# Optimization experiments

Hardware: AMD Instinct MI355X
Metric: run time of the kernel (lower is better)

The kernel has to match this reference:

```python
import jax, jax.numpy as jnp
import numpy as np

NUM_GRAPHS = 512

def setup_inputs() -> dict:
    key = jax.random.key(0)
    ks = jax.random.split(key, 6)
    N, E, D = 100000, 1600000, 128
    x = jax.random.normal(ks[0], (N, D), dtype=jnp.float32)
    edge_index = jax.random.randint(ks[1], (2, E), 0, N, dtype=jnp.int64)
    batch = jnp.sort(jax.random.randint(ks[2], (N,), 0, NUM_GRAPHS, dtype=jnp.int64))
    scale = 1.0 / np.sqrt(D)
    Ws = jax.random.normal(ks[3], (4, D, D), dtype=jnp.float32) * scale
    bs = jnp.zeros((4, D), dtype=jnp.float32)
    Wl = jax.random.normal(ks[4], (D, 1), dtype=jnp.float32) * scale
    bl = jnp.zeros((1,), dtype=jnp.float32)
    return {"x": x, "edge_index": edge_index, "batch": batch,
            "Ws": Ws, "bs": bs, "Wl": Wl, "bl": bl}

def reference(x, edge_index, batch, Ws, bs, Wl, bl):
    N = x.shape[0]
    loops = jnp.arange(N, dtype=edge_index.dtype)
    # GCNConv: add self-loops, symmetric normalization D^{-1/2} A D^{-1/2}
    row = jnp.concatenate([edge_index[0], loops])  # source nodes
    col = jnp.concatenate([edge_index[1], loops])  # target nodes
    deg = jax.ops.segment_sum(jnp.ones_like(col, dtype=x.dtype), col, num_segments=N)
    dinv = jnp.where(deg > 0, jax.lax.rsqrt(jnp.maximum(deg, 1.0)), 0.0)
    norm = dinv[row] * dinv[col]  # [E+N]
    h = x
    for i in range(Ws.shape[0]):
        h = h @ Ws[i]                                   # [N, D]
        msg = h[row] * norm[:, None]                    # gather + scale, [E+N, D]
        h = jax.ops.segment_sum(msg, col, num_segments=N) + bs[i]
        h = jax.nn.relu(h)                              # dropout is identity in eval
    # global_mean_pool over graphs
    sums = jax.ops.segment_sum(h, batch, num_segments=NUM_GRAPHS)
    cnt = jax.ops.segment_sum(jnp.ones((N,), h.dtype), batch, num_segments=NUM_GRAPHS)
    pooled = sums / jnp.maximum(cnt, 1.0)[:, None]      # [G, D]
    return pooled @ Wl + bl                             # [G, 1]
```

## Files before the change

kernel.cpp:

```cpp
#include <hip/hip_runtime.h>


constexpr int D = 128;
constexpr int NGRAPH = 512;
constexpr int CHUNK = 4096;
constexpr int BSH = 9;
constexpr int OP = 136;

typedef __attribute__((ext_vector_type(8))) short bf16x8;
typedef __attribute__((ext_vector_type(4))) float f32x4;
typedef int i32x4u __attribute__((ext_vector_type(4), aligned(4)));

__device__ __forceinline__ float bf2f(unsigned short b) {
    return __uint_as_float(((unsigned int)b) << 16);
}
__device__ __forceinline__ unsigned short f2bf(float f) {
    unsigned int u = __float_as_uint(f);
    u += 0x7FFFu + ((u >> 16) & 1u);
    return (unsigned short)(u >> 16);
}

__global__ __launch_bounds__(256) void setup_all(
        const float4* __restrict__ x4, ushort4* __restrict__ hb, int n4, int CB,
        const float* __restrict__ W, unsigned short* __restrict__ Wt,
        const int* __restrict__ ec, int E, int* __restrict__ bucketCnt) {
    __shared__ int h[256];
    const int t = threadIdx.x;
    const int b = blockIdx.x;
    if (b < CB) {
        int i = b * 256 + t;
        if (i < n4) {
            float4 v = x4[i];
            ushort4 o;
            o.x = f2bf(v.x); o.y = f2bf(v.y); o.z = f2bf(v.z); o.w = f2bf(v.w);
            hb[i] = o;
        }
    } else if (b < CB + 256) {
        int idx = (b - CB) * 256 + t;
        int i = idx >> 14;
        int rem = idx & 16383;
        int k = rem >> 7, c = rem & 127;
        Wt[(i << 14) + c * 128 + k] = f2bf(W[idx]);
    } else {
        h[t] = 0;
        __syncthreads();
        const int e0 = (b - CB - 256) * CHUNK;
        const int cnt = min(CHUNK, E - e0);
        for (int i = t; i < cnt; i += 256) atomicAdd(&h[ec[e0 + i] >> BSH], 1);
        __syncthreads();
        if (h[t]) atomicAdd(&bucketCnt[t], h[t]);
    }
}

__global__ __launch_bounds__(256) void bucket_scan(const int* __restrict__ bucketCnt,
                                                   int* __restrict__ bucketBase,
                                                   int* __restrict__ globCursor) {
    __shared__ int s[256];
    const int t = threadIdx.x;
    int v = bucketCnt[t];
    s[t] = v; __syncthreads();
    for (int off = 1; off < 256; off <<= 1) {
        int x = (t >= off) ? s[t - off] : 0;
        __syncthreads();
        s[t] += x;
        __syncthreads();
    }
    int excl = s[t] - v;
    bucketBase[t] = excl;
    globCursor[t] = excl;
}

__global__ __launch_bounds__(256) void scatter_pairs(const int* __restrict__ er,
                                                     const int* __restrict__ ec, int E,
                                                     int* __restrict__ globCursor,
                                                     int2* __restrict__ pairs) {
    __shared__ int h[256], lbase[256], cur[256], segd[256], s[256];
    __shared__ int2 stage[CHUNK];
    const int t = threadIdx.x;
    const int e0 = blockIdx.x * CHUNK;
    const int cnt = min(CHUNK, E - e0);

    h[t] = 0;
    __syncthreads();
    for (int i = t; i < cnt; i += 256) atomicAdd(&h[ec[e0 + i] >> BSH], 1);
    __syncthreads();
    int v = h[t];
    s[t] = v; __syncthreads();
    for (int off = 1; off < 256; off <<= 1) {
        int x = (t >= off) ? s[t - off] : 0;
        __syncthreads();
        s[t] += x;
        __syncthreads();
    }
    lbase[t] = s[t] - v;
    cur[t] = s[t] - v;
    segd[t] = atomicAdd(&globCursor[t], v) - lbase[t];
    __syncthreads();
    for (int i = t; i < cnt; i += 256) {
        int c = ec[e0 + i];
        int b = c >> BSH;
        int p = atomicAdd(&cur[b], 1);
        stage[p] = make_int2(er[e0 + i], c);
    }
    __syncthreads();
    for (int i = t; i < cnt; i += 256) {
        int2 pr = stage[i];
        int b = pr.y >> BSH;
        pairs[segd[b] + i] = pr;
    }
}

__global__ __launch_bounds__(256) void fill_csr(const int2* __restrict__ pairs,
                                                const int* __restrict__ bucketBase,
                                                const int* __restrict__ bucketCnt,
                                                int N, int E, int NBUCK,
                                                int* __restrict__ rowptr,
                                                float* __restrict__ dinv,
                                                int* __restrict__ srcs) {
    __shared__ int hist[512], lofs[512], s[256];
    const int t = threadIdx.x;
    const int b = blockIdx.x;
    const int c0 = b << BSH;
    const int base = bucketBase[b];
    const int cnt = bucketCnt[b];
    const int2* pp = pairs + base;

    hist[t] = 0; hist[t + 256] = 0;
    __syncthreads();
    for (int i = t; i < cnt; i += 256) atomicAdd(&hist[pp[i].y - c0], 1);
    __syncthreads();
    int a0 = hist[2 * t], a1 = hist[2 * t + 1];
    s[t] = a0 + a1; __syncthreads();
    for (int off = 1; off < 256; off <<= 1) {
        int x = (t >= off) ? s[t - off] : 0;
        __syncthreads();
        s[t] += x;
        __syncthreads();
    }
    int excl = s[t] - (a0 + a1);
    lofs[2 * t] = excl;
    lofs[2 * t + 1] = excl + a0;
    __syncthreads();
    const int nn = min(512, N - c0);
    for (int i = t; i < nn; i += 256) {
        rowptr[c0 + i] = base + lofs[i];
        dinv[c0 + i] = rsqrtf((float)hist[i] + 1.0f);
    }
    if (b == NBUCK - 1 && t == 0) rowptr[N] = E;
    __syncthreads();
    for (int i = t; i < cnt; i += 256) {
        int2 pr = pp[i];
        int p = atomicAdd(&lofs[pr.y - c0], 1);
        srcs[base + p] = pr.x;
    }
}

__global__ __launch_bounds__(256) void scale_x(uint4* __restrict__ Hb0,
                                               const float* __restrict__ dinv,
                                               int nq) {
    int i = blockIdx.x * 256 + threadIdx.x;
    if (i >= nq) return;
    float dv = dinv[i >> 4];
    uint4 v = Hb0[i];
    unsigned int* p = (unsigned int*)&v;
#pragma unroll
    for (int k = 0; k < 4; ++k) {
        unsigned int d = p[k];
        unsigned short lo = f2bf(bf2f((unsigned short)(d & 0xFFFFu)) * dv);
        unsigned short hi = f2bf(bf2f((unsigned short)(d >> 16)) * dv);
        p[k] = ((unsigned int)hi << 16) | lo;
    }
    Hb0[i] = v;
}

__global__ __launch_bounds__(256, 4) void layer_fused(
        const int* __restrict__ rowptr, const int* __restrict__ srcs,
        const float* __restrict__ dinv, const unsigned short* __restrict__ H,
        const unsigned short* __restrict__ Wt, const float* __restrict__ bias,
        unsigned short* __restrict__ Hn, float* __restrict__ dots,
        const float* __restrict__ Wl, int N, int writeDots) {
    __shared__ __align__(16) unsigned short u[4][16 * OP];
    const int wave = threadIdx.x >> 6;
    const int lane = threadIdx.x & 63;
    const int row16 = lane & 15;
    const int quad = lane >> 4;
    const int r0 = blockIdx.x * 64 + wave * 16;
    unsigned short* U = u[wave];
    const bf16x8* H8 = (const bf16x8*)H;
    const int gl = row16;

#pragma unroll 1
    for (int sstep = 0; sstep < 4; ++sstep) {
        const int rt = quad * 4 + sstep;
        const int row = r0 + rt;
        float acc[8] = {0.f, 0.f, 0.f, 0.f, 0.f, 0.f, 0.f, 0.f};
        float sn = 0.f;
        if (row < N) {
            sn = dinv[row];
            int j = rowptr[row];
            const int end = rowptr[row + 1];
            bf16x8 hv = H8[(size_t)row * 16 + gl];
#pragma unroll
            for (int k = 0; k < 8; ++k) acc[k] = bf2f((unsigned short)hv[k]);
            const int ne = end - j;
            const int nb = (ne + 7) >> 3;
            if (nb > 0) {
                i32x4u sA0, sA1, sB0, sB1;
                {
                    const i32x4u* sp = (const i32x4u*)(srcs + j);
                    sA0 = sp[0]; sA1 = sp[1];
                }
                if (nb > 1) {
                    const i32x4u* sp = (const i32x4u*)(srcs + j + 8);
                    sB0 = sp[0]; sB1 = sp[1];
                }
                bf16x8 hc[8], hn[8];
#pragma unroll
                for (int t = 0; t < 8; ++t) {
                    int idx = (t < 4) ? sA0[t] : sA1[t - 4];
                    int rr = (t < ne) ? idx : row;
                    hc[t] = H8[(size_t)rr * 16 + gl];
                }
#pragma unroll 1
                for (int b = 0; b < nb; ++b) {
                    if (b + 1 < nb) {
                        const int remn = ne - (b + 1) * 8;
                        int rn[8];
#pragma unroll
                        for (int t = 0; t < 8; ++t) {
                            int idx = (t < 4) ? sB0[t] : sB1[t - 4];
                            rn[t] = (t < remn) ? idx : row;
                        }
                        if (b + 2 < nb) {
                            const i32x4u* sp = (const i32x4u*)(srcs + j + (b + 2) * 8);
                            sB0 = sp[0]; sB1 = sp[1];
                        }
#pragma unroll
                        for (int t = 0; t < 8; ++t)
                            hn[t] = H8[(size_t)rn[t] * 16 + gl];
                    }
                    const int rem = ne - b * 8;
#pragma unroll
                    for (int t = 0; t < 8; ++t) {
                        const float w = (t < rem) ? 1.f : 0.f;
#pragma unroll
                        for (int k = 0; k < 8; ++k)
                            acc[k] = fmaf(w, bf2f((unsigned short)hc[t][k]), acc[k]);
                    }
#pragma unroll
                    for (int t = 0; t < 8; ++t) hc[t] = hn[t];
                }
            }
        }
        bf16x8 o;
#pragma unroll
        for (int k = 0; k < 8; ++k) o[k] = (short)f2bf(sn * acc[k]);
        *(bf16x8*)(U + rt * 128 + ((gl ^ rt) << 3)) = o;
    }

    bf16x8 a0[4];
#pragma unroll
    for (int kc = 0; kc < 4; ++kc) {
        const int ph = (kc * 4 + quad) ^ row16;
        a0[kc] = *(const bf16x8*)(U + row16 * 128 + ph * 8);
    }

    float dv[4];
    if (!writeDots) {
#pragma unroll
        for (int i = 0; i < 4; ++i) {
            int ra = r0 + quad * 4 + i;
            dv[i] = (ra < N) ? dinv[ra] : 0.f;
        }
    }

    float rd[4] = {0.f, 0.f, 0.f, 0.f};
#pragma unroll
    for (int ct = 0; ct < 8; ++ct) {
        const int col = ct * 16 + row16;
        const bf16x8* wc = (const bf16x8*)(Wt + (size_t)col * 128);
        f32x4 acc0 = {0.f, 0.f, 0.f, 0.f};
#pragma unroll
        for (int kc = 0; kc < 4; ++kc) {
            const bf16x8 wf = wc[kc * 4 + quad];
            acc0 = __builtin_amdgcn_mfma_f32_16x16x32_bf16(a0[kc], wf, acc0, 0, 0, 0);
        }
        const float bv = bias[col];
        if (writeDots) {
            const float wl = Wl[col];
#pragma unroll
            for (int i = 0; i < 4; ++i) rd[i] += fmaxf(acc0[i] + bv, 0.f) * wl;
        } else {
#pragma unroll
            for (int i = 0; i < 4; ++i)
                U[(quad * 4 + i) * OP + col] = f2bf(dv[i] * fmaxf(acc0[i] + bv, 0.f));
        }
    }

    if (writeDots) {
#pragma unroll
        for (int m = 1; m < 16; m <<= 1)
#pragma unroll
            for (int i = 0; i < 4; ++i) rd[i] += __shfl_xor(rd[i], m, 64);
        if (row16 == 0) {
#pragma unroll
            for (int i = 0; i < 4; ++i) dots[r0 + quad * 4 + i] = rd[i];
        }
    } else {
#pragma unroll
        for (int i = 0; i < 4; ++i) {
            int idx = i * 64 + lane;
            int row = idx >> 4, c8 = idx & 15;
            bf16x8 v = *(const bf16x8*)(U + row * OP + c8 * 8);
            *(bf16x8*)(Hn + (size_t)(r0 + row) * 128 + c8 * 8) = v;
        }
    }
}

__global__ __launch_bounds__(256) void pool_graphs(const float* __restrict__ dots,
                                                   const int* __restrict__ batch, int N,
                                                   const float* __restrict__ bl,
                                                   float* __restrict__ out) {
    __shared__ int bounds[2];
    __shared__ float red[4];
    const int g = blockIdx.x;
    const int t = threadIdx.x;
    if (t < 2) {
        int key = g + t;
        int lo = 0, hi = N;
        while (lo < hi) {
            int mid = (lo + hi) >> 1;
            if (batch[mid] < key) lo = mid + 1; else hi = mid;
        }
        bounds[t] = lo;
    }
    __syncthreads();
    const int lo = bounds[0], hi = bounds[1];
    float s = 0.f;
    for (int i = lo + t; i < hi; i += 256) s += dots[i];
#pragma unroll
    for (int off = 32; off > 0; off >>= 1) s += __shfl_down(s, off, 64);
    if ((t & 63) == 0) red[t >> 6] = s;
    __syncthreads();
    if (t == 0) {
        float tot = red[0] + red[1] + red[2] + red[3];
        int cnt = hi - lo;
        out[g] = tot / (float)(cnt > 0 ? cnt : 1) + bl[0];
    }
}

extern "C" void kernel_launch(void* const* d_in, const int* in_sizes, int n_in,
                              void* d_out, int out_size, void* d_ws, size_t ws_size,
                              hipStream_t stream) {
    const float* x     = (const float*)d_in[0];
    const int*   eidx  = (const int*)d_in[1];
    const int*   batch = (const int*)d_in[2];
    const float* Ws    = (const float*)d_in[3];
    const float* bs    = (const float*)d_in[4];
    const float* Wl    = (const float*)d_in[5];
    const float* bl    = (const float*)d_in[6];
    (void)n_in; (void)out_size;

    const int N = in_sizes[0] / D;
    const int E = in_sizes[1] / 2;
    const int* er = eidx;
    const int* ec = eidx + E;
    const int NBUCK = (N + 511) >> BSH;
    const int NCHUNK = (E + CHUNK - 1) / CHUNK;

    const int Npad = (N + 127) & ~127;
    const size_t hBytes = (size_t)Npad * D * sizeof(unsigned short);
    auto al = [](size_t v) { return (v + 255) & ~(size_t)255; };
    char* base = (char*)d_ws;
    size_t off = 0;

    unsigned short* Hb0 = (unsigned short*)base; off = al(hBytes);
    int* bucketCnt  = (int*)(base + off);
    int* globCursor = bucketCnt + 256;
    off = al(off + 512 * sizeof(int));
    int*   bucketBase = (int*)(base + off);  off = al(off + 256 * sizeof(int));
    float* dinv   = (float*)(base + off);    off = al(off + (size_t)Npad * sizeof(float));
    float* dots   = (float*)(base + off);    off = al(off + (size_t)Npad * sizeof(float));
    int*   rowptr = (int*)(base + off);      off = al(off + (size_t)(Npad + 64) * sizeof(int));
    int*   srcs   = (int*)(base + off);      off = al(off + (size_t)E * sizeof(int) + 64);
    unsigned short* Wt = (unsigned short*)(base + off);   off = al(off + 4 * 128 * 128 * sizeof(unsigned short));

    const bool twoBuf = ws_size >= off + hBytes;
    unsigned short* Hb1 = twoBuf ? (unsigned short*)(base + off)
                                 : (unsigned short*)d_in[0];
    int2* pairs = (int2*)Hb1;
    unsigned short* hb[2] = { Hb0, Hb1 };

    hipMemsetAsync(bucketCnt, 0, 256 * sizeof(int), stream);
    const int n4 = N * D / 4;
    const int CB = (n4 + 255) / 256;
    setup_all<<<CB + 256 + NCHUNK, 256, 0, stream>>>((const float4*)x, (ushort4*)Hb0,
                                                     n4, CB, Ws, Wt, ec, E, bucketCnt);

    bucket_scan<<<1, 256, 0, stream>>>(bucketCnt, bucketBase, globCursor);
    scatter_pairs<<<NCHUNK, 256, 0, stream>>>(er, ec, E, globCursor, pairs);
    fill_csr<<<NBUCK, 256, 0, stream>>>(pairs, bucketBase, bucketCnt, N, E, NBUCK,
                                        rowptr, dinv, srcs);
    const int nq = N * 16;
    scale_x<<<(nq + 255) / 256, 256, 0, stream>>>((uint4*)Hb0, dinv, nq);

    for (int i = 0; i < 4; ++i) {
        const unsigned short* Hc = hb[i & 1];
        unsigned short* Hn = hb[(i + 1) & 1];
        layer_fused<<<Npad / 64, 256, 0, stream>>>(rowptr, srcs, dinv, Hc,
                                                   Wt + (size_t)i * D * D,
                                                   bs + (size_t)i * D, Hn, dots, Wl,
                                                   N, (i == 3) ? 1 : 0);
    }

    pool_graphs<<<NGRAPH, 256, 0, stream>>>(dots, batch, N, bl, (float*)d_out);
}
```

Before: 486.0 us.

## Process two rows concurrently in aggregation and pack CSR build pairs into ints

```diff
diff --git a/kernel.cpp b/kernel.cpp
--- a/kernel.cpp
+++ b/kernel.cpp
@@ -73,9 +73,10 @@
 __global__ __launch_bounds__(256) void scatter_pairs(const int* __restrict__ er,
                                                      const int* __restrict__ ec, int E,
                                                      int* __restrict__ globCursor,
-                                                     int2* __restrict__ pairs) {
+                                                     int* __restrict__ pairs) {
     __shared__ int h[256], lbase[256], cur[256], segd[256], s[256];
-    __shared__ int2 stage[CHUNK];
+    __shared__ int stage[CHUNK];
+    __shared__ unsigned char sb[CHUNK];
     const int t = threadIdx.x;
     const int e0 = blockIdx.x * CHUNK;
     const int cnt = min(CHUNK, E - e0);
@@ -100,17 +101,17 @@
         int c = ec[e0 + i];
         int b = c >> BSH;
         int p = atomicAdd(&cur[b], 1);
-        stage[p] = make_int2(er[e0 + i], c);
+        stage[p] = (er[e0 + i] << BSH) | (c & 511);
+        sb[p] = (unsigned char)b;
     }
     __syncthreads();
     for (int i = t; i < cnt; i += 256) {
-        int2 pr = stage[i];
-        int b = pr.y >> BSH;
-        pairs[segd[b] + i] = pr;
-    }
-}
-
-__global__ __launch_bounds__(256) void fill_csr(const int2* __restrict__ pairs,
+        int b = sb[i];
+        pairs[segd[b] + i] = stage[i];
+    }
+}
+
+__global__ __launch_bounds__(256) void fill_csr(const int* __restrict__ pairs,
                                                 const int* __restrict__ bucketBase,
                                                 const int* __restrict__ bucketCnt,
                                                 int N, int E, int NBUCK,
@@ -123,11 +124,11 @@
     const int c0 = b << BSH;
     const int base = bucketBase[b];
     const int cnt = bucketCnt[b];
-    const int2* pp = pairs + base;
+    const int* pp = pairs + base;
 
     hist[t] = 0; hist[t + 256] = 0;
     __syncthreads();
-    for (int i = t; i < cnt; i += 256) atomicAdd(&hist[pp[i].y - c0], 1);
+    for (int i = t; i < cnt; i += 256) atomicAdd(&hist[pp[i] & 511], 1);
     __syncthreads();
     int a0 = hist[2 * t], a1 = hist[2 * t + 1];
     s[t] = a0 + a1; __syncthreads();
@@ -149,9 +150,9 @@
     if (b == NBUCK - 1 && t == 0) rowptr[N] = E;
     __syncthreads();
     for (int i = t; i < cnt; i += 256) {
-        int2 pr = pp[i];
-        int p = atomicAdd(&lofs[pr.y - c0], 1);
-        srcs[base + p] = pr.x;
+        int pr = pp[i];
+        int p = atomicAdd(&lofs[pr & 511], 1);
+        srcs[base + p] = pr >> BSH;
     }
 }
 
@@ -173,7 +174,7 @@
     Hb0[i] = v;
 }
 
-__global__ __launch_bounds__(256, 4) void layer_fused(
+__global__ __launch_bounds__(256, 3) void layer_fused(
         const int* __restrict__ rowptr, const int* __restrict__ srcs,
         const float* __restrict__ dinv, const unsigned short* __restrict__ H,
         const unsigned short* __restrict__ Wt, const float* __restrict__ bias,
@@ -190,72 +191,75 @@
     const int gl = row16;
 
 #pragma unroll 1
-    for (int sstep = 0; sstep < 4; ++sstep) {
-        const int rt = quad * 4 + sstep;
-        const int row = r0 + rt;
-        float acc[8] = {0.f, 0.f, 0.f, 0.f, 0.f, 0.f, 0.f, 0.f};
-        float sn = 0.f;
-        if (row < N) {
-            sn = dinv[row];
-            int j = rowptr[row];
-            const int end = rowptr[row + 1];
-            bf16x8 hv = H8[(size_t)row * 16 + gl];
-#pragma unroll
-            for (int k = 0; k < 8; ++k) acc[k] = bf2f((unsigned short)hv[k]);
-            const int ne = end - j;
-            const int nb = (ne + 7) >> 3;
-            if (nb > 0) {
-                i32x4u sA0, sA1, sB0, sB1;
-                {
-                    const i32x4u* sp = (const i32x4u*)(srcs + j);
-                    sA0 = sp[0]; sA1 = sp[1];
+    for (int ss = 0; ss < 2; ++ss) {
+        const int rtA = quad * 4 + ss * 2, rtB = rtA + 1;
+        const int rowA = r0 + rtA, rowB = r0 + rtB;
+        const int selfA = min(rowA, N - 1), selfB = min(rowB, N - 1);
+        const float snA = (rowA < N) ? dinv[rowA] : 0.f;
+        const float snB = (rowB < N) ? dinv[rowB] : 0.f;
+        int jA = 0, neA = 0, jB = 0, neB = 0;
+        if (rowA < N) { jA = rowptr[rowA]; neA = rowptr[rowA + 1] - jA; }
+        if (rowB < N) { jB = rowptr[rowB]; neB = rowptr[rowB + 1] - jB; }
+        float accA[8], accB[8];
+        {
+            bf16x8 hvA = H8[(size_t)selfA * 16 + gl];
+            bf16x8 hvB = H8[(size_t)selfB * 16 + gl];
+#pragma unroll
+            for (int k = 0; k < 8; ++k) {
+                accA[k] = bf2f((unsigned short)hvA[k]);
+                accB[k] = bf2f((unsigned short)hvB[k]);
+            }
+        }
+        const int nbA = (neA + 3) >> 2, nbB = (neB + 3) >> 2;
+        const int nb = max(nbA, nbB);
+        if (nb > 0) {
+            i32x4u sAc = {0, 0, 0, 0}, sBc = {0, 0, 0, 0};
+            i32x4u sAn = {0, 0, 0, 0}, sBn = {0, 0, 0, 0};
+            if (nbA > 0) sAc = *(const i32x4u*)(srcs + jA);
+            if (nbB > 0) sBc = *(const i32x4u*)(srcs + jB);
+            if (nbA > 1) sAn = *(const i32x4u*)(srcs + jA + 4);
+            if (nbB > 1) sBn = *(const i32x4u*)(srcs + jB + 4);
+            bf16x8 hA[4], hB[4], hAn[4], hBn[4];
+#pragma unroll
+            for (int t = 0; t < 4; ++t) {
+                hA[t] = H8[(size_t)((t < neA) ? sAc[t] : selfA) * 16 + gl];
+                hB[t] = H8[(size_t)((t < neB) ? sBc[t] : selfB) * 16 + gl];
+            }
+#pragma unroll 1
+            for (int b = 0; b < nb; ++b) {
+                if (b + 1 < nb) {
+                    const int bn = (b + 1) * 4;
+#pragma unroll
+                    for (int t = 0; t < 4; ++t) {
+                        hAn[t] = H8[(size_t)((bn + t < neA) ? sAn[t] : selfA) * 16 + gl];
+                        hBn[t] = H8[(size_t)((bn + t < neB) ? sBn[t] : selfB) * 16 + gl];
+                    }
+                    if (b + 2 < nbA) sAn = *(const i32x4u*)(srcs + jA + (b + 2) * 4);
+                    if (b + 2 < nbB) sBn = *(const i32x4u*)(srcs + jB + (b + 2) * 4);
                 }
-                if (nb > 1) {
-                    const i32x4u* sp = (const i32x4u*)(srcs + j + 8);
-                    sB0 = sp[0]; sB1 = sp[1];
+                const int rb = b * 4;
+#pragma unroll
+                for (int t = 0; t < 4; ++t) {
+                    const float wA = (rb + t < neA) ? 1.f : 0.f;
+                    const float wB = (rb + t < neB) ? 1.f : 0.f;
+#pragma unroll
+                    for (int k = 0; k < 8; ++k) {
+                        accA[k] = fmaf(wA, bf2f((unsigned short)hA[t][k]), accA[k]);
+                        accB[k] = fmaf(wB, bf2f((unsigned short)hB[t][k]), accB[k]);
+                    }
                 }
-                bf16x8 hc[8], hn[8];
-#pragma unroll
-                for (int t = 0; t < 8; ++t) {
-                    int idx = (t < 4) ? sA0[t] : sA1[t - 4];
-                    int rr = (t < ne) ? idx : row;
-                    hc[t] = H8[(size_t)rr * 16 + gl];
-                }
-#pragma unroll 1
-                for (int b = 0; b < nb; ++b) {
-                    if (b + 1 < nb) {
-                        const int remn = ne - (b + 1) * 8;
-                        int rn[8];
-#pragma unroll
-                        for (int t = 0; t < 8; ++t) {
-                            int idx = (t < 4) ? sB0[t] : sB1[t - 4];
-                            rn[t] = (t < remn) ? idx : row;
-                        }
-                        if (b + 2 < nb) {
-                            const i32x4u* sp = (const i32x4u*)(srcs + j + (b + 2) * 8);
-                            sB0 = sp[0]; sB1 = sp[1];
-                        }
-#pragma unroll
-                        for (int t = 0; t < 8; ++t)
-                            hn[t] = H8[(size_t)rn[t] * 16 + gl];
-                    }
-                    const int rem = ne - b * 8;
-#pragma unroll
-                    for (int t = 0; t < 8; ++t) {
-                        const float w = (t < rem) ? 1.f : 0.f;
-#pragma unroll
-                        for (int k = 0; k < 8; ++k)
-                            acc[k] = fmaf(w, bf2f((unsigned short)hc[t][k]), acc[k]);
-                    }
-#pragma unroll
-                    for (int t = 0; t < 8; ++t) hc[t] = hn[t];
-                }
+#pragma unroll
+                for (int t = 0; t < 4; ++t) { hA[t] = hAn[t]; hB[t] = hBn[t]; }
             }
         }
-        bf16x8 o;
-#pragma unroll
-        for (int k = 0; k < 8; ++k) o[k] = (short)f2bf(sn * acc[k]);
-        *(bf16x8*)(U + rt * 128 + ((gl ^ rt) << 3)) = o;
+        bf16x8 oA, oB;
+#pragma unroll
+        for (int k = 0; k < 8; ++k) {
+            oA[k] = (short)f2bf(snA * accA[k]);
+            oB[k] = (short)f2bf(snB * accB[k]);
+        }
+        *(bf16x8*)(U + rtA * 128 + ((gl ^ rtA) << 3)) = oA;
+        *(bf16x8*)(U + rtB * 128 + ((gl ^ rtB) << 3)) = oB;
     }
 
     bf16x8 a0[4];
@@ -388,7 +392,7 @@
     const bool twoBuf = ws_size >= off + hBytes;
     unsigned short* Hb1 = twoBuf ? (unsigned short*)(base + off)
                                  : (unsigned short*)d_in[0];
-    int2* pairs = (int2*)Hb1;
+    int* pairs = (int*)Hb1;
     unsigned short* hb[2] = { Hb0, Hb1 };
 
     hipMemsetAsync(bucketCnt, 0, 256 * sizeof(int), stream);
```

Result: slower. 520.7 us (+7.1%).

## Pad CSR rows to multiples of eight with sentinel and pack edge pairs

Applied to the files above, without the earlier changes.

```diff
diff --git a/kernel.cpp b/kernel.cpp
--- a/kernel.cpp
+++ b/kernel.cpp
@@ -3,8 +3,9 @@
 
 constexpr int D = 128;
 constexpr int NGRAPH = 512;
-constexpr int CHUNK = 4096;
+constexpr int CHUNK = 2048;
 constexpr int BSH = 9;
+constexpr int SLACK = 4096;
 constexpr int OP = 136;
 
 typedef __attribute__((ext_vector_type(8))) short bf16x8;
@@ -73,9 +74,10 @@
 __global__ __launch_bounds__(256) void scatter_pairs(const int* __restrict__ er,
                                                      const int* __restrict__ ec, int E,
                                                      int* __restrict__ globCursor,
-                                                     int2* __restrict__ pairs) {
+                                                     int* __restrict__ pairs) {
     __shared__ int h[256], lbase[256], cur[256], segd[256], s[256];
-    __shared__ int2 stage[CHUNK];
+    __shared__ int stage[CHUNK];
+    __shared__ unsigned char sb[CHUNK];
     const int t = threadIdx.x;
     const int e0 = blockIdx.x * CHUNK;
     const int cnt = min(CHUNK, E - e0);
@@ -100,59 +102,72 @@
         int c = ec[e0 + i];
         int b = c >> BSH;
         int p = atomicAdd(&cur[b], 1);
-        stage[p] = make_int2(er[e0 + i], c);
+        stage[p] = (er[e0 + i] << BSH) | (c & 511);
+        sb[p] = (unsigned char)b;
     }
     __syncthreads();
     for (int i = t; i < cnt; i += 256) {
-        int2 pr = stage[i];
-        int b = pr.y >> BSH;
-        pairs[segd[b] + i] = pr;
-    }
-}
-
-__global__ __launch_bounds__(256) void fill_csr(const int2* __restrict__ pairs,
+        int b = sb[i];
+        pairs[segd[b] + i] = stage[i];
+    }
+}
+
+__global__ __launch_bounds__(256) void fill_csr(const int* __restrict__ pairs,
                                                 const int* __restrict__ bucketBase,
                                                 const int* __restrict__ bucketCnt,
                                                 int N, int E, int NBUCK,
-                                                int* __restrict__ rowptr,
+                                                int* __restrict__ rowbeg,
+                                                int* __restrict__ nbatch,
                                                 float* __restrict__ dinv,
                                                 int* __restrict__ srcs) {
     __shared__ int hist[512], lofs[512], s[256];
+    __shared__ int ptotS;
     const int t = threadIdx.x;
     const int b = blockIdx.x;
     const int c0 = b << BSH;
     const int base = bucketBase[b];
     const int cnt = bucketCnt[b];
-    const int2* pp = pairs + base;
+    const int pbase = base + b * SLACK;
+    const int* pp = pairs + base;
 
     hist[t] = 0; hist[t + 256] = 0;
     __syncthreads();
-    for (int i = t; i < cnt; i += 256) atomicAdd(&hist[pp[i].y - c0], 1);
-    __syncthreads();
-    int a0 = hist[2 * t], a1 = hist[2 * t + 1];
-    s[t] = a0 + a1; __syncthreads();
+    for (int i = t; i < cnt; i += 256) atomicAdd(&hist[pp[i] & 511], 1);
+    __syncthreads();
+    const int a0 = hist[2 * t], a1 = hist[2 * t + 1];
+    const int p0 = (a0 + 7) & ~7, p1 = (a1 + 7) & ~7;
+    s[t] = p0 + p1; __syncthreads();
     for (int off = 1; off < 256; off <<= 1) {
         int x = (t >= off) ? s[t - off] : 0;
         __syncthreads();
         s[t] += x;
         __syncthreads();
     }
-    int excl = s[t] - (a0 + a1);
+    const int excl = s[t] - (p0 + p1);
+    if (t == 255) ptotS = s[255];
     lofs[2 * t] = excl;
-    lofs[2 * t + 1] = excl + a0;
+    lofs[2 * t + 1] = excl + p0;
     __syncthreads();
     const int nn = min(512, N - c0);
     for (int i = t; i < nn; i += 256) {
-        rowptr[c0 + i] = base + lofs[i];
+        rowbeg[c0 + i] = pbase + lofs[i];
+        nbatch[c0 + i] = (hist[i] + 7) >> 3;
         dinv[c0 + i] = rsqrtf((float)hist[i] + 1.0f);
     }
-    if (b == NBUCK - 1 && t == 0) rowptr[N] = E;
     __syncthreads();
     for (int i = t; i < cnt; i += 256) {
-        int2 pr = pp[i];
-        int p = atomicAdd(&lofs[pr.y - c0], 1);
-        srcs[base + p] = pr.x;
-    }
+        int pr = pp[i];
+        int p = atomicAdd(&lofs[pr & 511], 1);
+        srcs[pbase + p] = pr >> BSH;
+    }
+    {
+        int s0 = excl;
+        for (int q = a0; q < p0; ++q) srcs[pbase + s0 + q] = N;
+        int s1 = excl + p0;
+        for (int q = a1; q < p1; ++q) srcs[pbase + s1 + q] = N;
+    }
+    const int ptot = ptotS;
+    for (int q = ptot + t; q < cnt + SLACK; q += 256) srcs[pbase + q] = N;
 }
 
 __global__ __launch_bounds__(256) void scale_x(uint4* __restrict__ Hb0,
@@ -173,8 +188,9 @@
     Hb0[i] = v;
 }
 
-__global__ __launch_bounds__(256, 4) void layer_fused(
-        const int* __restrict__ rowptr, const int* __restrict__ srcs,
+__global__ __launch_bounds__(256, 2) void layer_fused(
+        const int* __restrict__ rowbeg, const int* __restrict__ nbatch,
+        const int* __restrict__ srcs,
         const float* __restrict__ dinv, const unsigned short* __restrict__ H,
         const unsigned short* __restrict__ Wt, const float* __restrict__ bias,
         unsigned short* __restrict__ Hn, float* __restrict__ dots,
@@ -189,67 +205,58 @@
     const bf16x8* H8 = (const bf16x8*)H;
     const int gl = row16;
 
+    int rowP = r0 + quad * 4;
+    int jrN = 0, nbN = 0; float snN = 0.f;
+    if (rowP < N) { jrN = rowbeg[rowP]; nbN = nbatch[rowP]; snN = dinv[rowP]; }
 #pragma unroll 1
     for (int sstep = 0; sstep < 4; ++sstep) {
         const int rt = quad * 4 + sstep;
         const int row = r0 + rt;
+        const int jr = jrN, nb = nbN;
+        const float sn = snN;
+        if (sstep < 3) {
+            const int rn = row + 1;
+            if (rn < N) { jrN = rowbeg[rn]; nbN = nbatch[rn]; snN = dinv[rn]; }
+            else { jrN = 0; nbN = 0; snN = 0.f; }
+        }
         float acc[8] = {0.f, 0.f, 0.f, 0.f, 0.f, 0.f, 0.f, 0.f};
-        float sn = 0.f;
         if (row < N) {
-            sn = dinv[row];
-            int j = rowptr[row];
-            const int end = rowptr[row + 1];
             bf16x8 hv = H8[(size_t)row * 16 + gl];
 #pragma unroll
             for (int k = 0; k < 8; ++k) acc[k] = bf2f((unsigned short)hv[k]);
-            const int ne = end - j;
-            const int nb = (ne + 7) >> 3;
             if (nb > 0) {
-                i32x4u sA0, sA1, sB0, sB1;
-                {
-                    const i32x4u* sp = (const i32x4u*)(srcs + j);
-                    sA0 = sp[0]; sA1 = sp[1];
+                i32x4u sB0 = *(const i32x4u*)(srcs + jr);
+                i32x4u sB1 = *(const i32x4u*)(srcs + jr + 4);
+                bf16x8 h[8], hn[8];
+#pragma unroll
+                for (int t = 0; t < 8; ++t) {
+                    int idx = (t < 4) ? sB0[t] : sB1[t - 4];
+                    h[t] = H8[(size_t)idx * 16 + gl];
                 }
-                if (nb > 1) {
-                    const i32x4u* sp = (const i32x4u*)(srcs + j + 8);
-                    sB0 = sp[0]; sB1 = sp[1];
+                sB0 = *(const i32x4u*)(srcs + jr + 8);
+                sB1 = *(const i32x4u*)(srcs + jr + 12);
+#pragma unroll 1
+                for (int b = 0; b < nb - 1; ++b) {
+#pragma unroll
+                    for (int t = 0; t < 8; ++t) {
+                        int idx = (t < 4) ? sB0[t] : sB1[t - 4];
+                        hn[t] = H8[(size_t)idx * 16 + gl];
+                    }
+                    sB0 = *(const i32x4u*)(srcs + jr + (b + 2) * 8);
+                    sB1 = *(const i32x4u*)(srcs + jr + (b + 2) * 8 + 4);
+#pragma unroll
+                    for (int t = 0; t < 8; ++t)
+#pragma unroll
+                        for (int k = 0; k < 8; ++k)
+                            acc[k] += bf2f((unsigned short)h[t][k]);
+#pragma unroll
+                    for (int t = 0; t < 8; ++t) h[t] = hn[t];
                 }
-                bf16x8 hc[8], hn[8];
-#pragma unroll
-                for (int t = 0; t < 8; ++t) {
-                    int idx = (t < 4) ? sA0[t] : sA1[t - 4];
-                    int rr = (t < ne) ? idx : row;
-                    hc[t] = H8[(size_t)rr * 16 + gl];
-                }
-#pragma unroll 1
-                for (int b = 0; b < nb; ++b) {
-                    if (b + 1 < nb) {
-                        const int remn = ne - (b + 1) * 8;
-                        int rn[8];
-#pragma unroll
-                        for (int t = 0; t < 8; ++t) {
-                            int idx = (t < 4) ? sB0[t] : sB1[t - 4];
-                            rn[t] = (t < remn) ? idx : row;
-                        }
-                        if (b + 2 < nb) {
-                            const i32x4u* sp = (const i32x4u*)(srcs + j + (b + 2) * 8);
-                            sB0 = sp[0]; sB1 = sp[1];
-                        }
-#pragma unroll
-                        for (int t = 0; t < 8; ++t)
-                            hn[t] = H8[(size_t)rn[t] * 16 + gl];
-                    }
-                    const int rem = ne - b * 8;
-#pragma unroll
-                    for (int t = 0; t < 8; ++t) {
-                        const float w = (t < rem) ? 1.f : 0.f;
-#pragma unroll
-                        for (int k = 0; k < 8; ++k)
-                            acc[k] = fmaf(w, bf2f((unsigned short)hc[t][k]), acc[k]);
-                    }
-#pragma unroll
-                    for (int t = 0; t < 8; ++t) hc[t] = hn[t];
-                }
+#pragma unroll
+                for (int t = 0; t < 8; ++t)
+#pragma unroll
+                    for (int k = 0; k < 8; ++k)
+                        acc[k] += bf2f((unsigned short)h[t][k]);
             }
         }
         bf16x8 o;
@@ -381,17 +388,20 @@
     int*   bucketBase = (int*)(base + off);  off = al(off + 256 * sizeof(int));
     float* dinv   = (float*)(base + off);    off = al(off + (size_t)Npad * sizeof(float));
     float* dots   = (float*)(base + off);    off = al(off + (size_t)Npad * sizeof(float));
-    int*   rowptr = (int*)(base + off);      off = al(off + (size_t)(Npad + 64) * sizeof(int));
-    int*   srcs   = (int*)(base + off);      off = al(off + (size_t)E * sizeof(int) + 64);
+    int*   rowbeg = (int*)(base + off);      off = al(off + (size_t)Npad * sizeof(int));
+    int*   nbatch = (int*)(base + off);      off = al(off + (size_t)Npad * sizeof(int));
+    int*   srcs   = (int*)(base + off);
+    off = al(off + ((size_t)E + (size_t)NBUCK * SLACK + 64) * sizeof(int));
     unsigned short* Wt = (unsigned short*)(base + off);   off = al(off + 4 * 128 * 128 * sizeof(unsigned short));
 
     const bool twoBuf = ws_size >= off + hBytes;
     unsigned short* Hb1 = twoBuf ? (unsigned short*)(base + off)
                                  : (unsigned short*)d_in[0];
-    int2* pairs = (int2*)Hb1;
+    int* pairs = (int*)Hb1;
     unsigned short* hb[2] = { Hb0, Hb1 };
 
     hipMemsetAsync(bucketCnt, 0, 256 * sizeof(int), stream);
+    hipMemsetAsync(Hb0 + (size_t)N * D, 0, (size_t)(Npad - N) * D * sizeof(unsigned short), stream);
     const int n4 = N * D / 4;
     const int CB = (n4 + 255) / 256;
     setup_all<<<CB + 256 + NCHUNK, 256, 0, stream>>>((const float4*)x, (ushort4*)Hb0,
@@ -400,14 +410,14 @@
     bucket_scan<<<1, 256, 0, stream>>>(bucketCnt, bucketBase, globCursor);
     scatter_pairs<<<NCHUNK, 256, 0, stream>>>(er, ec, E, globCursor, pairs);
     fill_csr<<<NBUCK, 256, 0, stream>>>(pairs, bucketBase, bucketCnt, N, E, NBUCK,
-                                        rowptr, dinv, srcs);
+                                        rowbeg, nbatch, dinv, srcs);
     const int nq = N * 16;
     scale_x<<<(nq + 255) / 256, 256, 0, stream>>>((uint4*)Hb0, dinv, nq);
 
     for (int i = 0; i < 4; ++i) {
         const unsigned short* Hc = hb[i & 1];
         unsigned short* Hn = hb[(i + 1) & 1];
-        layer_fused<<<Npad / 64, 256, 0, stream>>>(rowptr, srcs, dinv, Hc,
+        layer_fused<<<Npad / 64, 256, 0, stream>>>(rowbeg, nbatch, srcs, dinv, Hc,
                                                    Wt + (size_t)i * D * D,
                                                    bs + (size_t)i * D, Hn, dots, Wl,
                                                    N, (i == 3) ? 1 : 0);
```

Result: slower. 511.2 us (+5.2%).

## Pack edge pairs into one int, use single-wave layer blocks, simplify gather loop

Applied to the files above, without the earlier changes.

```diff
diff --git a/kernel.cpp b/kernel.cpp
--- a/kernel.cpp
+++ b/kernel.cpp
@@ -3,7 +3,7 @@
 
 constexpr int D = 128;
 constexpr int NGRAPH = 512;
-constexpr int CHUNK = 4096;
+constexpr int CHUNK = 2048;
 constexpr int BSH = 9;
 constexpr int OP = 136;
 
@@ -73,9 +73,10 @@
 __global__ __launch_bounds__(256) void scatter_pairs(const int* __restrict__ er,
                                                      const int* __restrict__ ec, int E,
                                                      int* __restrict__ globCursor,
-                                                     int2* __restrict__ pairs) {
+                                                     int* __restrict__ pairs) {
     __shared__ int h[256], lbase[256], cur[256], segd[256], s[256];
-    __shared__ int2 stage[CHUNK];
+    __shared__ int stage[CHUNK];
+    __shared__ unsigned char sb[CHUNK];
     const int t = threadIdx.x;
     const int e0 = blockIdx.x * CHUNK;
     const int cnt = min(CHUNK, E - e0);
@@ -100,17 +101,17 @@
         int c = ec[e0 + i];
         int b = c >> BSH;
         int p = atomicAdd(&cur[b], 1);
-        stage[p] = make_int2(er[e0 + i], c);
+        stage[p] = (er[e0 + i] << BSH) | (c & 511);
+        sb[p] = (unsigned char)b;
     }
     __syncthreads();
     for (int i = t; i < cnt; i += 256) {
-        int2 pr = stage[i];
-        int b = pr.y >> BSH;
-        pairs[segd[b] + i] = pr;
-    }
-}
-
-__global__ __launch_bounds__(256) void fill_csr(const int2* __restrict__ pairs,
+        int b = sb[i];
+        pairs[segd[b] + i] = stage[i];
+    }
+}
+
+__global__ __launch_bounds__(256) void fill_csr(const int* __restrict__ pairs,
                                                 const int* __restrict__ bucketBase,
                                                 const int* __restrict__ bucketCnt,
                                                 int N, int E, int NBUCK,
@@ -123,11 +124,11 @@
     const int c0 = b << BSH;
     const int base = bucketBase[b];
     const int cnt = bucketCnt[b];
-    const int2* pp = pairs + base;
+    const int* pp = pairs + base;
 
     hist[t] = 0; hist[t + 256] = 0;
     __syncthreads();
-    for (int i = t; i < cnt; i += 256) atomicAdd(&hist[pp[i].y - c0], 1);
+    for (int i = t; i < cnt; i += 256) atomicAdd(&hist[pp[i] & 511], 1);
     __syncthreads();
     int a0 = hist[2 * t], a1 = hist[2 * t + 1];
     s[t] = a0 + a1; __syncthreads();
@@ -149,9 +150,9 @@
     if (b == NBUCK - 1 && t == 0) rowptr[N] = E;
     __syncthreads();
     for (int i = t; i < cnt; i += 256) {
-        int2 pr = pp[i];
-        int p = atomicAdd(&lofs[pr.y - c0], 1);
-        srcs[base + p] = pr.x;
+        int pr = pp[i];
+        int p = atomicAdd(&lofs[pr & 511], 1);
+        srcs[base + p] = pr >> BSH;
     }
 }
 
@@ -173,19 +174,17 @@
     Hb0[i] = v;
 }
 
-__global__ __launch_bounds__(256, 4) void layer_fused(
+__global__ __launch_bounds__(64, 4) void layer_fused(
         const int* __restrict__ rowptr, const int* __restrict__ srcs,
         const float* __restrict__ dinv, const unsigned short* __restrict__ H,
         const unsigned short* __restrict__ Wt, const float* __restrict__ bias,
         unsigned short* __restrict__ Hn, float* __restrict__ dots,
         const float* __restrict__ Wl, int N, int writeDots) {
-    __shared__ __align__(16) unsigned short u[4][16 * OP];
-    const int wave = threadIdx.x >> 6;
-    const int lane = threadIdx.x & 63;
+    __shared__ __align__(16) unsigned short U[16 * OP];
+    const int lane = threadIdx.x;
     const int row16 = lane & 15;
     const int quad = lane >> 4;
-    const int r0 = blockIdx.x * 64 + wave * 16;
-    unsigned short* U = u[wave];
+    const int r0 = blockIdx.x * 16;
     const bf16x8* H8 = (const bf16x8*)H;
     const int gl = row16;
 
@@ -197,58 +196,51 @@
         float sn = 0.f;
         if (row < N) {
             sn = dinv[row];
-            int j = rowptr[row];
-            const int end = rowptr[row + 1];
+            const int j = rowptr[row];
+            const int ne = rowptr[row + 1] - j;
             bf16x8 hv = H8[(size_t)row * 16 + gl];
 #pragma unroll
             for (int k = 0; k < 8; ++k) acc[k] = bf2f((unsigned short)hv[k]);
-            const int ne = end - j;
             const int nb = (ne + 7) >> 3;
             if (nb > 0) {
-                i32x4u sA0, sA1, sB0, sB1;
-                {
-                    const i32x4u* sp = (const i32x4u*)(srcs + j);
-                    sA0 = sp[0]; sA1 = sp[1];
+                i32x4u s0 = *(const i32x4u*)(srcs + j);
+                i32x4u s1 = *(const i32x4u*)(srcs + j + 4);
+                bf16x8 h[8], hn[8];
+#pragma unroll
+                for (int t = 0; t < 8; ++t) {
+                    int idx = (t < 4) ? s0[t] : s1[t - 4];
+                    int rr = (t < ne) ? idx : row;
+                    h[t] = H8[(size_t)rr * 16 + gl];
                 }
-                if (nb > 1) {
-                    const i32x4u* sp = (const i32x4u*)(srcs + j + 8);
-                    sB0 = sp[0]; sB1 = sp[1];
+                s0 = *(const i32x4u*)(srcs + j + 8);
+                s1 = *(const i32x4u*)(srcs + j + 12);
+#pragma unroll 1
+                for (int b = 0; b + 1 < nb; ++b) {
+                    const int remn = ne - (b + 1) * 8;
+#pragma unroll
+                    for (int t = 0; t < 8; ++t) {
+                        int idx = (t < 4) ? s0[t] : s1[t - 4];
+                        int rr = (t < remn) ? idx : row;
+                        hn[t] = H8[(size_t)rr * 16 + gl];
+                    }
+                    s0 = *(const i32x4u*)(srcs + j + (b + 2) * 8);
+                    s1 = *(const i32x4u*)(srcs + j + (b + 2) * 8 + 4);
+                    __builtin_amdgcn_sched_barrier(0);
+#pragma unroll
+                    for (int t = 0; t < 8; ++t)
+#pragma unroll
+                        for (int k = 0; k < 8; ++k)
+                            acc[k] += bf2f((unsigned short)h[t][k]);
+#pragma unroll
+                    for (int t = 0; t < 8; ++t) h[t] = hn[t];
                 }
-                bf16x8 hc[8], hn[8];
+                const int rem = ne - (nb - 1) * 8;
 #pragma unroll
                 for (int t = 0; t < 8; ++t) {
-                    int idx = (t < 4) ? sA0[t] : sA1[t - 4];
-                    int rr = (t < ne) ? idx : row;
-                    hc[t] = H8[(size_t)rr * 16 + gl];
-                }
-#pragma unroll 1
-                for (int b = 0; b < nb; ++b) {
-                    if (b + 1 < nb) {
-                        const int remn = ne - (b + 1) * 8;
-                        int rn[8];
-#pragma unroll
-                        for (int t = 0; t < 8; ++t) {
-                            int idx = (t < 4) ? sB0[t] : sB1[t - 4];
-                            rn[t] = (t < remn) ? idx : row;
-                        }
-                        if (b + 2 < nb) {
-                            const i32x4u* sp = (const i32x4u*)(srcs + j + (b + 2) * 8);
-                            sB0 = sp[0]; sB1 = sp[1];
-                        }
-#pragma unroll
-                        for (int t = 0; t < 8; ++t)
-                            hn[t] = H8[(size_t)rn[t] * 16 + gl];
-                    }
-                    const int rem = ne - b * 8;
-#pragma unroll
-                    for (int t = 0; t < 8; ++t) {
-                        const float w = (t < rem) ? 1.f : 0.f;
-#pragma unroll
-                        for (int k = 0; k < 8; ++k)
-                            acc[k] = fmaf(w, bf2f((unsigned short)hc[t][k]), acc[k]);
-                    }
-#pragma unroll
-                    for (int t = 0; t < 8; ++t) hc[t] = hn[t];
+                    const float w = (t < rem) ? 1.f : 0.f;
+#pragma unroll
+                    for (int k = 0; k < 8; ++k)
+                        acc[k] = fmaf(w, bf2f((unsigned short)h[t][k]), acc[k]);
                 }
             }
         }
@@ -257,6 +249,7 @@
         for (int k = 0; k < 8; ++k) o[k] = (short)f2bf(sn * acc[k]);
         *(bf16x8*)(U + rt * 128 + ((gl ^ rt) << 3)) = o;
     }
+    __syncthreads();
 
     bf16x8 a0[4];
 #pragma unroll
@@ -264,6 +257,7 @@
         const int ph = (kc * 4 + quad) ^ row16;
         a0[kc] = *(const bf16x8*)(U + row16 * 128 + ph * 8);
     }
+    __syncthreads();
 
     float dv[4];
     if (!writeDots) {
@@ -307,6 +301,7 @@
             for (int i = 0; i < 4; ++i) dots[r0 + quad * 4 + i] = rd[i];
         }
     } else {
+        __syncthreads();
 #pragma unroll
         for (int i = 0; i < 4; ++i) {
             int idx = i * 64 + lane;
@@ -382,13 +377,13 @@
     float* dinv   = (float*)(base + off);    off = al(off + (size_t)Npad * sizeof(float));
     float* dots   = (float*)(base + off);    off = al(off + (size_t)Npad * sizeof(float));
     int*   rowptr = (int*)(base + off);      off = al(off + (size_t)(Npad + 64) * sizeof(int));
-    int*   srcs   = (int*)(base + off);      off = al(off + (size_t)E * sizeof(int) + 64);
+    int*   srcs   = (int*)(base + off);      off = al(off + ((size_t)E + 64) * sizeof(int));
     unsigned short* Wt = (unsigned short*)(base + off);   off = al(off + 4 * 128 * 128 * sizeof(unsigned short));
 
     const bool twoBuf = ws_size >= off + hBytes;
     unsigned short* Hb1 = twoBuf ? (unsigned short*)(base + off)
                                  : (unsigned short*)d_in[0];
-    int2* pairs = (int2*)Hb1;
+    int* pairs = (int*)Hb1;
     unsigned short* hb[2] = { Hb0, Hb1 };
 
     hipMemsetAsync(bucketCnt, 0, 256 * sizeof(int), stream);
@@ -407,10 +402,10 @@
     for (int i = 0; i < 4; ++i) {
         const unsigned short* Hc = hb[i & 1];
         unsigned short* Hn = hb[(i + 1) & 1];
-        layer_fused<<<Npad / 64, 256, 0, stream>>>(rowptr, srcs, dinv, Hc,
-                                                   Wt + (size_t)i * D * D,
-                                                   bs + (size_t)i * D, Hn, dots, Wl,
-                                                   N, (i == 3) ? 1 : 0);
+        layer_fused<<<Npad / 16, 64, 0, stream>>>(rowptr, srcs, dinv, Hc,
+                                                  Wt + (size_t)i * D * D,
+                                                  bs + (size_t)i * D, Hn, dots, Wl,
+                                                  N, (i == 3) ? 1 : 0);
     }
 
     pool_graphs<<<NGRAPH, 256, 0, stream>>>(dots, batch, N, bl, (float*)d_out);
```

Result: no change. 490.0 us (+0.8%).
